# Performance work log

Measured on AMD Instinct MI355X. Metric: run time of the kernel, lower is better.

The kernel has to match this reference:

```python
import jax, jax.numpy as jnp
import numpy as np

NB_OBJECTS = 3
DIM_BODY = 10
DIM_OBJECT = 15
DIM_OBJ_FEAT = NB_OBJECTS + DIM_OBJECT  # 18
DIM_PHI_IN = 54
HID = 256
DIM_PHI_OUT = 256
DIM_RHO_OUT = 1
B = 65536

# (o1, o2) object pair and (j, k) predicate indices, as in the torch code
PAIRS = [((0, 1), (3, 5)), ((0, 2), (4, 7)), ((1, 2), (6, 8))]


def setup_inputs() -> dict:
    key = jax.random.key(0)
    ks = jax.random.split(key, 24)
    inp = {
        "obs": jax.random.normal(ks[0], (B, 55), dtype=jnp.float32),
        "ag": jax.random.uniform(ks[1], (B, 9), dtype=jnp.float32),
        "g": jax.random.uniform(ks[2], (B, 9), dtype=jnp.float32),
        "anchor_g": jax.random.uniform(ks[3], (B, 9), dtype=jnp.float32),
        "act": jax.random.normal(ks[4], (B, 4), dtype=jnp.float32),
    }
    s = 0.05
    # PhiCriticDeepSet: two independent 2-layer MLPs (streams 1 and 2)
    inp["w1"] = jax.random.normal(ks[5], (DIM_PHI_IN, HID), dtype=jnp.float32) * s
    inp["b1"] = jnp.zeros((HID,), dtype=jnp.float32)
    inp["w2"] = jax.random.normal(ks[6], (HID, DIM_PHI_OUT), dtype=jnp.float32) * s
    inp["b2"] = jnp.zeros((DIM_PHI_OUT,), dtype=jnp.float32)
    inp["w3"] = jax.random.normal(ks[7], (DIM_PHI_IN, HID), dtype=jnp.float32) * s
    inp["b3"] = jnp.zeros((HID,), dtype=jnp.float32)
    inp["w4"] = jax.random.normal(ks[8], (HID, DIM_PHI_OUT), dtype=jnp.float32) * s
    inp["b4"] = jnp.zeros((DIM_PHI_OUT,), dtype=jnp.float32)
    # RhoCriticDeepSet: two independent 2-layer heads
    inp["w5"] = jax.random.normal(ks[9], (DIM_PHI_OUT, HID), dtype=jnp.float32) * s
    inp["b5"] = jnp.zeros((HID,), dtype=jnp.float32)
    inp["w6"] = jax.random.normal(ks[10], (HID, DIM_RHO_OUT), dtype=jnp.float32) * s
    inp["b6"] = jnp.zeros((DIM_RHO_OUT,), dtype=jnp.float32)
    inp["w7"] = jax.random.normal(ks[11], (DIM_PHI_OUT, HID), dtype=jnp.float32) * s
    inp["b7"] = jnp.zeros((HID,), dtype=jnp.float32)
    inp["w8"] = jax.random.normal(ks[12], (HID, DIM_RHO_OUT), dtype=jnp.float32) * s
    inp["b8"] = jnp.zeros((DIM_RHO_OUT,), dtype=jnp.float32)
    return inp


def _build_pair_inputs(obs, ag, g, act, anchor_g):
    """combinations_trick branch: data-dependent gather of goal bits and object pairs."""
    bs = obs.shape[0]
    obs_body = obs[:, :DIM_BODY]
    eye = jnp.eye(NB_OBJECTS, dtype=obs.dtype)
    # obs_objects: [3, B, 18] = one-hot(3) ++ object state(15)
    obs_objects = jnp.stack([
        jnp.concatenate([jnp.broadcast_to(eye[i], (bs, NB_OBJECTS)),
                         obs[:, DIM_BODY + DIM_OBJECT * i: DIM_BODY + DIM_OBJECT * (i + 1)]],
                        axis=1)
        for i in range(NB_OBJECTS)], axis=0)
    bidx = jnp.arange(bs)
    inputs = []
    for i, ((o1, o2), (j, k)) in enumerate(PAIRS):
        # selector = anchor_g @ [e_j, e_k] difference = anchor_g[:, j] - anchor_g[:, k]
        sel = (anchor_g[:, j] - anchor_g[:, k]) >= 0  # [B] bool
        # idxs_bits[i] = [i, j] where sel else [i, k]
        bit2 = jnp.where(sel, j, k)  # [B] int
        ag_pair = jnp.stack([ag[:, i], ag[bidx, bit2]], axis=1)  # [B, 2]
        g_pair = jnp.stack([g[:, i], g[bidx, bit2]], axis=1)     # [B, 2]
        # idxs_objects[i] = [o1, o2] where sel else [o2, o1]
        oi = jnp.where(sel, o1, o2)  # [B]
        oj = jnp.where(sel, o2, o1)
        obj_first = obs_objects[oi, bidx]   # [B, 18] gather along object axis
        obj_second = obs_objects[oj, bidx]  # [B, 18]
        inputs.append(jnp.concatenate(
            [ag_pair, g_pair, obs_body, obj_first, obj_second, act], axis=1))
    return jnp.stack(inputs)  # [3, B, 54]


def reference(obs, ag, g, anchor_g, act,
              w1, b1, w2, b2, w3, b3, w4, b4,
              w5, b5, w6, b6, w7, b7, w8, b8):
    inp = _build_pair_inputs(obs, ag, g, act, anchor_g)  # [3, B, 54]
    # PhiCriticDeepSet (two relu-relu streams)
    x1 = jax.nn.relu(jnp.einsum('pbi,ih->pbh', jax.nn.relu(jnp.einsum('pbd,dh->pbh', inp, w1) + b1), w2) + b2)
    x2 = jax.nn.relu(jnp.einsum('pbi,ih->pbh', jax.nn.relu(jnp.einsum('pbd,dh->pbh', inp, w3) + b3), w4) + b4)
    s1 = x1.sum(axis=0)  # [B, 256] deepset sum over pairs
    s2 = x2.sum(axis=0)
    # RhoCriticDeepSet readouts
    q1 = jax.nn.relu(s1 @ w5 + b5) @ w6 + b6  # [B, 1]
    q2 = jax.nn.relu(s2 @ w7 + b7) @ w8 + b8  # [B, 1]
    return (q1, q2)
```

## Files before the change

### kernel.cpp

```cpp
#include <hip/hip_runtime.h>
#include <hip/hip_bf16.h>

typedef unsigned short u16;
typedef unsigned int   u32;

using bf8 = __attribute__((ext_vector_type(8))) __bf16;
using f4  = __attribute__((ext_vector_type(4))) float;

__device__ __forceinline__ float b2f(u16 u) {
    union { u32 i; float f; } v; v.i = ((u32)u) << 16; return v.f;
}
__device__ __forceinline__ u16 f2b(float f) {
    union { float f; u32 i; } v; v.f = f;
    u32 x = v.i;
    x += 0x7fffu + ((x >> 16) & 1u);
    return (u16)(x >> 16);
}
__device__ __forceinline__ u32 pk2(float lo, float hi) {
    union { __hip_bfloat162 h; u32 u; } v;
    v.h = __float22bfloat162_rn(make_float2(lo, hi));
    return v.u;
}

__global__ void swz_all(const float* __restrict__ w1, const float* __restrict__ w3,
                        const float* __restrict__ w2, const float* __restrict__ w4,
                        const float* __restrict__ w5, const float* __restrict__ w7,
                        u16* __restrict__ ws) {
    __shared__ u16 slab[32 * 270];
    int b = blockIdx.x, t = threadIdx.x;
    const float* src; u16* dst; int kmax, kt;
    if      (b <  2) { src = w1; dst = ws;          kmax = 54;  kt = b;      }
    else if (b <  4) { src = w3; dst = ws + 16384;  kmax = 54;  kt = b - 2;  }
    else if (b < 12) { src = w2; dst = ws + 32768;  kmax = 256; kt = b - 4;  }
    else if (b < 20) { src = w4; dst = ws + 98304;  kmax = 256; kt = b - 12; }
    else if (b < 28) { src = w5; dst = ws + 163840; kmax = 256; kt = b - 20; }
    else             { src = w7; dst = ws + 229376; kmax = 256; kt = b - 28; }

    #pragma unroll
    for (int it = 0; it < 8; ++it) {
        int flat = it * 1024 + t * 4;
        int row = flat >> 8, col = flat & 255;
        int k = kt * 32 + row;
        float4 v = make_float4(0.f, 0.f, 0.f, 0.f);
        if (k < kmax) v = *(const float4*)(src + k * 256 + col);
        u32* sp = (u32*)&slab[row * 270 + col];
        sp[0] = pk2(v.x, v.y);
        sp[1] = pk2(v.z, v.w);
    }
    __syncthreads();

    int lane = t & 63, wave = t >> 6, lr = lane & 15, kg = lane >> 4;
    #pragma unroll
    for (int i = 0; i < 4; ++i) {
        int ct = wave * 4 + i;
        u16 v[8];
        #pragma unroll
        for (int j = 0; j < 8; ++j)
            v[j] = slab[(kg * 8 + j) * 270 + ct * 16 + lr];
        uint4 o;
        o.x = (u32)v[0] | ((u32)v[1] << 16);
        o.y = (u32)v[2] | ((u32)v[3] << 16);
        o.z = (u32)v[4] | ((u32)v[5] << 16);
        o.w = (u32)v[6] | ((u32)v[7] << 16);
        *(uint4*)(dst + (size_t)(((kt * 16 + ct) * 64 + lane) * 8)) = o;
    }
}

#define HS    264
#define H_OFF 3456
#define S2O   (16 * HS)
#define RH0O  (32 * HS)

__global__ __launch_bounds__(256, 2) void critic_kernel(
    const float* __restrict__ obs, const float* __restrict__ ag,
    const float* __restrict__ g,   const float* __restrict__ anchor,
    const float* __restrict__ act,
    const float* __restrict__ b1,  const float* __restrict__ b2,
    const float* __restrict__ b3,  const float* __restrict__ b4,
    const float* __restrict__ b5,  const float* __restrict__ b7,
    const float* __restrict__ w6,  const float* __restrict__ b6,
    const float* __restrict__ w8,  const float* __restrict__ b8,
    const u16* __restrict__ wsz, float* __restrict__ out, int B) {

    __shared__ u16 pool[H_OFF + 48 * HS];

    const int t    = threadIdx.x;
    const int lane = t & 63;
    const int wave = t >> 6;
    const int lr   = lane & 15;
    const int lg   = lane >> 4;
    const int wg   = blockIdx.x;

    if (t < 48) {
        const int O1[3] = {0, 0, 1}, O2[3] = {1, 2, 2};
        const int JA[3] = {3, 4, 6}, KA[3] = {5, 7, 8};
        int p = t / 16, bl = t % 16;
        int b = wg * 16 + bl;
        int j = JA[p], k = KA[p];
        bool sel = (anchor[b * 9 + j] - anchor[b * 9 + k]) >= 0.0f;
        int bit2 = sel ? j : k;
        int oi = sel ? O1[p] : O2[p];
        int oj = sel ? O2[p] : O1[p];
        u16* row = &pool[t * 72];
        row[0] = f2b(ag[b * 9 + p]);
        row[1] = f2b(ag[b * 9 + bit2]);
        row[2] = f2b(g[b * 9 + p]);
        row[3] = f2b(g[b * 9 + bit2]);
        for (int c = 0; c < 10; ++c) row[4 + c] = f2b(obs[b * 55 + c]);
        const u16 ONE = 0x3F80;
        row[14] = (oi == 0) ? ONE : 0; row[15] = (oi == 1) ? ONE : 0; row[16] = (oi == 2) ? ONE : 0;
        for (int c = 0; c < 15; ++c) row[17 + c] = f2b(obs[b * 55 + 10 + 15 * oi + c]);
        row[32] = (oj == 0) ? ONE : 0; row[33] = (oj == 1) ? ONE : 0; row[34] = (oj == 2) ? ONE : 0;
        for (int c = 0; c < 15; ++c) row[35 + c] = f2b(obs[b * 55 + 10 + 15 * oj + c]);
        for (int c = 0; c < 4; ++c)  row[50 + c] = f2b(act[b * 4 + c]);
        for (int c = 54; c < 64; ++c) row[c] = 0;
    }
    __syncthreads();

    u32 s1w[4][2];
    u32 s2w[4][2];

    for (int net = 0; net < 2; ++net) {
        const u16* Wl1 = wsz + (net ? 16384 : 0);
        const u16* Wl2 = wsz + 32768 + (net ? 65536 : 0);
        const float* bl1 = net ? b3 : b1;
        const float* bl2 = net ? b4 : b2;

        f4 acc[3][4];
        #pragma unroll
        for (int rt = 0; rt < 3; ++rt)
            #pragma unroll
            for (int c = 0; c < 4; ++c) acc[rt][c] = (f4){0.f, 0.f, 0.f, 0.f};
        #pragma unroll
        for (int kt = 0; kt < 2; ++kt) {
            bf8 wfr[4];
            #pragma unroll
            for (int c = 0; c < 4; ++c)
                wfr[c] = *(const bf8*)(Wl1 + (size_t)(((kt * 16 + wave * 4 + c) * 64 + lane) * 8));
            #pragma unroll
            for (int rt = 0; rt < 3; ++rt) {
                bf8 xfr = *(const bf8*)(&pool[(rt * 16 + lr) * 72 + kt * 32 + lg * 8]);
                #pragma unroll
                for (int c = 0; c < 4; ++c)
                    acc[rt][c] = __builtin_amdgcn_mfma_f32_16x16x32_bf16(wfr[c], xfr, acc[rt][c], 0, 0, 0);
            }
        }
        #pragma unroll
        for (int c = 0; c < 4; ++c) {
            float4 bv = *(const float4*)(bl1 + (wave * 4 + c) * 16 + lg * 4);
            #pragma unroll
            for (int rt = 0; rt < 3; ++rt) {
                uint2 w;
                w.x = pk2(fmaxf(acc[rt][c][0] + bv.x, 0.f), fmaxf(acc[rt][c][1] + bv.y, 0.f));
                w.y = pk2(fmaxf(acc[rt][c][2] + bv.z, 0.f), fmaxf(acc[rt][c][3] + bv.w, 0.f));
                *(uint2*)&pool[H_OFF + (rt * 16 + lr) * HS + (wave * 4 + c) * 16 + lg * 4] = w;
            }
        }
        __syncthreads();

        f4 acc2[3][4];
        #pragma unroll
        for (int rt = 0; rt < 3; ++rt)
            #pragma unroll
            for (int c = 0; c < 4; ++c) acc2[rt][c] = (f4){0.f, 0.f, 0.f, 0.f};
        #pragma unroll
        for (int ks = 0; ks < 8; ++ks) {
            bf8 wfr[4];
            #pragma unroll
            for (int c = 0; c < 4; ++c)
                wfr[c] = *(const bf8*)(Wl2 + (size_t)(((ks * 16 + wave * 4 + c) * 64 + lane) * 8));
            #pragma unroll
            for (int rt = 0; rt < 3; ++rt) {
                bf8 hfr = *(const bf8*)(&pool[H_OFF + (rt * 16 + lr) * HS + ks * 32 + lg * 8]);
                #pragma unroll
                for (int c = 0; c < 4; ++c)
                    acc2[rt][c] = __builtin_amdgcn_mfma_f32_16x16x32_bf16(wfr[c], hfr, acc2[rt][c], 0, 0, 0);
            }
        }
        #pragma unroll
        for (int c = 0; c < 4; ++c) {
            float4 bv = *(const float4*)(bl2 + (wave * 4 + c) * 16 + lg * 4);
            f4 sv = (f4){0.f, 0.f, 0.f, 0.f};
            #pragma unroll
            for (int p = 0; p < 3; ++p) {
                sv[0] += fmaxf(acc2[p][c][0] + bv.x, 0.f);
                sv[1] += fmaxf(acc2[p][c][1] + bv.y, 0.f);
                sv[2] += fmaxf(acc2[p][c][2] + bv.z, 0.f);
                sv[3] += fmaxf(acc2[p][c][3] + bv.w, 0.f);
            }
            if (net == 0) {
                s1w[c][0] = pk2(sv[0], sv[1]);
                s1w[c][1] = pk2(sv[2], sv[3]);
            } else {
                s2w[c][0] = pk2(sv[0], sv[1]);
                s2w[c][1] = pk2(sv[2], sv[3]);
            }
        }
        __syncthreads();
    }

    #pragma unroll
    for (int c = 0; c < 4; ++c) {
        int base = H_OFF + lr * HS + (wave * 4 + c) * 16 + lg * 4;
        *(uint2*)&pool[base]       = *(uint2*)&s1w[c][0];
        *(uint2*)&pool[base + S2O] = *(uint2*)&s2w[c][0];
    }
    __syncthreads();

    {
        const u16* W5 = wsz + 163840;
        const u16* W7 = wsz + 229376;
        f4 racc[2][4];
        #pragma unroll
        for (int rt = 0; rt < 2; ++rt)
            #pragma unroll
            for (int c = 0; c < 4; ++c) racc[rt][c] = (f4){0.f, 0.f, 0.f, 0.f};
        #pragma unroll
        for (int ks = 0; ks < 8; ++ks) {
            bf8 w5f[4], w7f[4];
            #pragma unroll
            for (int c = 0; c < 4; ++c) {
                size_t off = (size_t)(((ks * 16 + wave * 4 + c) * 64 + lane) * 8);
                w5f[c] = *(const bf8*)(W5 + off);
                w7f[c] = *(const bf8*)(W7 + off);
            }
            bf8 s1f = *(const bf8*)(&pool[H_OFF + lr * HS + ks * 32 + lg * 8]);
            bf8 s2f = *(const bf8*)(&pool[H_OFF + S2O + lr * HS + ks * 32 + lg * 8]);
            #pragma unroll
            for (int c = 0; c < 4; ++c) {
                racc[0][c] = __builtin_amdgcn_mfma_f32_16x16x32_bf16(w5f[c], s1f, racc[0][c], 0, 0, 0);
                racc[1][c] = __builtin_amdgcn_mfma_f32_16x16x32_bf16(w7f[c], s2f, racc[1][c], 0, 0, 0);
            }
        }
        #pragma unroll
        for (int c = 0; c < 4; ++c) {
            float4 bv = *(const float4*)(b5 + (wave * 4 + c) * 16 + lg * 4);
            uint2 w;
            w.x = pk2(fmaxf(racc[0][c][0] + bv.x, 0.f), fmaxf(racc[0][c][1] + bv.y, 0.f));
            w.y = pk2(fmaxf(racc[0][c][2] + bv.z, 0.f), fmaxf(racc[0][c][3] + bv.w, 0.f));
            *(uint2*)&pool[H_OFF + RH0O + lr * HS + (wave * 4 + c) * 16 + lg * 4] = w;
        }
        __syncthreads();
        #pragma unroll
        for (int c = 0; c < 4; ++c) {
            float4 bv = *(const float4*)(b7 + (wave * 4 + c) * 16 + lg * 4);
            uint2 w;
            w.x = pk2(fmaxf(racc[1][c][0] + bv.x, 0.f), fmaxf(racc[1][c][1] + bv.y, 0.f));
            w.y = pk2(fmaxf(racc[1][c][2] + bv.z, 0.f), fmaxf(racc[1][c][3] + bv.w, 0.f));
            *(uint2*)&pool[H_OFF + lr * HS + (wave * 4 + c) * 16 + lg * 4] = w;
        }
        __syncthreads();
    }

    {
        int oidx = t & 31;
        int kc   = t >> 5;
        int net  = oidx >> 4, r = oidx & 15;
        int hoff = net ? H_OFF : H_OFF + RH0O;
        const float* wv = net ? w8 : w6;
        float s = 0.f;
        int base = hoff + r * HS + kc * 32;
        #pragma unroll
        for (int it = 0; it < 8; ++it) {
            uint2 two = *(const uint2*)&pool[base + it * 4];
            float4 wq = *(const float4*)(wv + kc * 32 + it * 4);
            s += __uint_as_float(two.x << 16)          * wq.x;
            s += __uint_as_float(two.x & 0xffff0000u)  * wq.y;
            s += __uint_as_float(two.y << 16)          * wq.z;
            s += __uint_as_float(two.y & 0xffff0000u)  * wq.w;
        }
        __syncthreads();
        ((u32*)pool)[t] = __float_as_uint(s);
    }
    __syncthreads();
    if (t < 32) {
        int net = t >> 4, r = t & 15;
        float qv = net ? b8[0] : b6[0];
        #pragma unroll
        for (int kc = 0; kc < 8; ++kc)
            qv += __uint_as_float(((u32*)pool)[kc * 32 + t]);
        out[net * B + wg * 16 + r] = qv;
    }
}

extern "C" void kernel_launch(void* const* d_in, const int* in_sizes, int n_in,
                              void* d_out, int out_size, void* d_ws, size_t ws_size,
                              hipStream_t stream) {
    const float* obs = (const float*)d_in[0];
    const float* ag  = (const float*)d_in[1];
    const float* g   = (const float*)d_in[2];
    const float* anc = (const float*)d_in[3];
    const float* act = (const float*)d_in[4];
    const float* w1  = (const float*)d_in[5];
    const float* b1  = (const float*)d_in[6];
    const float* w2  = (const float*)d_in[7];
    const float* b2  = (const float*)d_in[8];
    const float* w3  = (const float*)d_in[9];
    const float* b3  = (const float*)d_in[10];
    const float* w4  = (const float*)d_in[11];
    const float* b4  = (const float*)d_in[12];
    const float* w5  = (const float*)d_in[13];
    const float* b5  = (const float*)d_in[14];
    const float* w6  = (const float*)d_in[15];
    const float* b6  = (const float*)d_in[16];
    const float* w7  = (const float*)d_in[17];
    const float* b7  = (const float*)d_in[18];
    const float* w8  = (const float*)d_in[19];
    const float* b8  = (const float*)d_in[20];
    u16* ws    = (u16*)d_ws;
    float* out = (float*)d_out;
    int B = in_sizes[0] / 55;

    swz_all<<<36, 256, 0, stream>>>(w1, w3, w2, w4, w5, w7, ws);
    critic_kernel<<<(B + 15) / 16, 256, 0, stream>>>(obs, ag, g, anc, act,
                                                     b1, b2, b3, b4, b5, b7,
                                                     w6, b6, w8, b8, ws, out, B);
}
```

Before: 228.4 us.

## Process two 16-row batch tiles per block with software-pipelined stages

Each workgroup now handles 32 batch rows as two 16-row halves and interleaves their stages (layer1 of one half with layer2 of the other, rho with dot products) across shared barriers. This halves the number of barriers per row and lets independent MFMA work from two tiles overlap with LDS writes and global weight fetches. The cost is roughly double the LDS footprint and more live registers, which may reduce occupancy under the 2-blocks launch bound, and half as many blocks are launched.

```diff
diff --git a/kernel.cpp b/kernel.cpp
--- a/kernel.cpp
+++ b/kernel.cpp
@@ -66,10 +66,166 @@
     }
 }
 
-#define HS    264
-#define H_OFF 3456
-#define S2O   (16 * HS)
-#define RH0O  (32 * HS)
+#define HS   264
+#define HA   6912
+#define HB   19584
+
+__device__ __forceinline__ void do_l1(u16* pool, int lane, int wave, int lr, int lg,
+                                      const u16* W, const float* bias,
+                                      int inpOff, int hOff) {
+    f4 acc[3][4];
+    #pragma unroll
+    for (int rt = 0; rt < 3; ++rt)
+        #pragma unroll
+        for (int c = 0; c < 4; ++c) acc[rt][c] = (f4){0.f, 0.f, 0.f, 0.f};
+    #pragma unroll
+    for (int kt = 0; kt < 2; ++kt) {
+        bf8 wfr[4];
+        #pragma unroll
+        for (int c = 0; c < 4; ++c)
+            wfr[c] = *(const bf8*)(W + (size_t)(((kt * 16 + wave * 4 + c) * 64 + lane) * 8));
+        #pragma unroll
+        for (int rt = 0; rt < 3; ++rt) {
+            bf8 xfr = *(const bf8*)(&pool[inpOff + (rt * 16 + lr) * 72 + kt * 32 + lg * 8]);
+            #pragma unroll
+            for (int c = 0; c < 4; ++c)
+                acc[rt][c] = __builtin_amdgcn_mfma_f32_16x16x32_bf16(wfr[c], xfr, acc[rt][c], 0, 0, 0);
+        }
+    }
+    #pragma unroll
+    for (int c = 0; c < 4; ++c) {
+        float4 bv = *(const float4*)(bias + (wave * 4 + c) * 16 + lg * 4);
+        #pragma unroll
+        for (int rt = 0; rt < 3; ++rt) {
+            uint2 w;
+            w.x = pk2(fmaxf(acc[rt][c][0] + bv.x, 0.f), fmaxf(acc[rt][c][1] + bv.y, 0.f));
+            w.y = pk2(fmaxf(acc[rt][c][2] + bv.z, 0.f), fmaxf(acc[rt][c][3] + bv.w, 0.f));
+            *(uint2*)&pool[hOff + (rt * 16 + lr) * HS + (wave * 4 + c) * 16 + lg * 4] = w;
+        }
+    }
+}
+
+__device__ __forceinline__ void do_l2(u16* pool, int lane, int wave, int lr, int lg,
+                                      const u16* W, const float* bias,
+                                      int hOff, u32 sw[4][2]) {
+    f4 acc2[3][4];
+    #pragma unroll
+    for (int rt = 0; rt < 3; ++rt)
+        #pragma unroll
+        for (int c = 0; c < 4; ++c) acc2[rt][c] = (f4){0.f, 0.f, 0.f, 0.f};
+    #pragma unroll
+    for (int ks = 0; ks < 8; ++ks) {
+        bf8 wfr[4];
+        #pragma unroll
+        for (int c = 0; c < 4; ++c)
+            wfr[c] = *(const bf8*)(W + (size_t)(((ks * 16 + wave * 4 + c) * 64 + lane) * 8));
+        #pragma unroll
+        for (int rt = 0; rt < 3; ++rt) {
+            bf8 hfr = *(const bf8*)(&pool[hOff + (rt * 16 + lr) * HS + ks * 32 + lg * 8]);
+            #pragma unroll
+            for (int c = 0; c < 4; ++c)
+                acc2[rt][c] = __builtin_amdgcn_mfma_f32_16x16x32_bf16(wfr[c], hfr, acc2[rt][c], 0, 0, 0);
+        }
+    }
+    #pragma unroll
+    for (int c = 0; c < 4; ++c) {
+        float4 bv = *(const float4*)(bias + (wave * 4 + c) * 16 + lg * 4);
+        f4 sv = (f4){0.f, 0.f, 0.f, 0.f};
+        #pragma unroll
+        for (int p = 0; p < 3; ++p) {
+            sv[0] += fmaxf(acc2[p][c][0] + bv.x, 0.f);
+            sv[1] += fmaxf(acc2[p][c][1] + bv.y, 0.f);
+            sv[2] += fmaxf(acc2[p][c][2] + bv.z, 0.f);
+            sv[3] += fmaxf(acc2[p][c][3] + bv.w, 0.f);
+        }
+        sw[c][0] = pk2(sv[0], sv[1]);
+        sw[c][1] = pk2(sv[2], sv[3]);
+    }
+}
+
+__device__ __forceinline__ void do_swrite(u16* pool, int wave, int lr, int lg,
+                                          int sOff, u32 s1[4][2], u32 s2[4][2]) {
+    #pragma unroll
+    for (int c = 0; c < 4; ++c) {
+        int base = sOff + lr * HS + (wave * 4 + c) * 16 + lg * 4;
+        *(uint2*)&pool[base]           = *(uint2*)&s1[c][0];
+        *(uint2*)&pool[base + 16 * HS] = *(uint2*)&s2[c][0];
+    }
+}
+
+__device__ __forceinline__ void do_rho(u16* pool, int lane, int wave, int lr, int lg,
+                                       const u16* W5, const u16* W7,
+                                       const float* b5, const float* b7,
+                                       int sOff, int rh0Off, int rh1Off) {
+    f4 racc[2][4];
+    #pragma unroll
+    for (int rt = 0; rt < 2; ++rt)
+        #pragma unroll
+        for (int c = 0; c < 4; ++c) racc[rt][c] = (f4){0.f, 0.f, 0.f, 0.f};
+    #pragma unroll
+    for (int ks = 0; ks < 8; ++ks) {
+        bf8 w5f[4], w7f[4];
+        #pragma unroll
+        for (int c = 0; c < 4; ++c) {
+            size_t off = (size_t)(((ks * 16 + wave * 4 + c) * 64 + lane) * 8);
+            w5f[c] = *(const bf8*)(W5 + off);
+            w7f[c] = *(const bf8*)(W7 + off);
+        }
+        bf8 s1f = *(const bf8*)(&pool[sOff + lr * HS + ks * 32 + lg * 8]);
+        bf8 s2f = *(const bf8*)(&pool[sOff + 16 * HS + lr * HS + ks * 32 + lg * 8]);
+        #pragma unroll
+        for (int c = 0; c < 4; ++c) {
+            racc[0][c] = __builtin_amdgcn_mfma_f32_16x16x32_bf16(w5f[c], s1f, racc[0][c], 0, 0, 0);
+            racc[1][c] = __builtin_amdgcn_mfma_f32_16x16x32_bf16(w7f[c], s2f, racc[1][c], 0, 0, 0);
+        }
+    }
+    #pragma unroll
+    for (int c = 0; c < 4; ++c) {
+        float4 bv5 = *(const float4*)(b5 + (wave * 4 + c) * 16 + lg * 4);
+        float4 bv7 = *(const float4*)(b7 + (wave * 4 + c) * 16 + lg * 4);
+        uint2 w0, w1;
+        w0.x = pk2(fmaxf(racc[0][c][0] + bv5.x, 0.f), fmaxf(racc[0][c][1] + bv5.y, 0.f));
+        w0.y = pk2(fmaxf(racc[0][c][2] + bv5.z, 0.f), fmaxf(racc[0][c][3] + bv5.w, 0.f));
+        w1.x = pk2(fmaxf(racc[1][c][0] + bv7.x, 0.f), fmaxf(racc[1][c][1] + bv7.y, 0.f));
+        w1.y = pk2(fmaxf(racc[1][c][2] + bv7.z, 0.f), fmaxf(racc[1][c][3] + bv7.w, 0.f));
+        int col = (wave * 4 + c) * 16 + lg * 4;
+        *(uint2*)&pool[rh0Off + lr * HS + col] = w0;
+        *(uint2*)&pool[rh1Off + lr * HS + col] = w1;
+    }
+}
+
+__device__ __forceinline__ void do_dotpart(u16* pool, int t,
+                                           const float* w6, const float* w8,
+                                           int rh0Off, int rh1Off, int partOff) {
+    int oidx = t & 31, kc = t >> 5;
+    int net = oidx >> 4, r = oidx & 15;
+    const float* wv = net ? w8 : w6;
+    int base = (net ? rh1Off : rh0Off) + r * HS + kc * 32;
+    float s = 0.f;
+    #pragma unroll
+    for (int it = 0; it < 8; ++it) {
+        uint2 two = *(const uint2*)&pool[base + it * 4];
+        float4 wq = *(const float4*)(wv + kc * 32 + it * 4);
+        s += __uint_as_float(two.x << 16)          * wq.x;
+        s += __uint_as_float(two.x & 0xffff0000u)  * wq.y;
+        s += __uint_as_float(two.y << 16)          * wq.z;
+        s += __uint_as_float(two.y & 0xffff0000u)  * wq.w;
+    }
+    ((u32*)pool)[partOff + t] = __float_as_uint(s);
+}
+
+__device__ __forceinline__ void do_out(u16* pool, int t,
+                                       const float* b6, const float* b8,
+                                       int partOff, float* out, int bbase, int B) {
+    if (t < 32) {
+        int net = t >> 4, r = t & 15;
+        float qv = net ? b8[0] : b6[0];
+        #pragma unroll
+        for (int kc = 0; kc < 8; ++kc)
+            qv += __uint_as_float(((u32*)pool)[partOff + kc * 32 + t]);
+        out[net * B + bbase + r] = qv;
+    }
+}
 
 __global__ __launch_bounds__(256, 2) void critic_kernel(
     const float* __restrict__ obs, const float* __restrict__ ag,
@@ -82,7 +238,7 @@
     const float* __restrict__ w8,  const float* __restrict__ b8,
     const u16* __restrict__ wsz, float* __restrict__ out, int B) {
 
-    __shared__ u16 pool[H_OFF + 48 * HS];
+    __shared__ u16 pool[6912 + 96 * HS];
 
     const int t    = threadIdx.x;
     const int lane = t & 63;
@@ -91,17 +247,26 @@
     const int lg   = lane >> 4;
     const int wg   = blockIdx.x;
 
-    if (t < 48) {
+    const u16* W1n0 = wsz;
+    const u16* W1n1 = wsz + 16384;
+    const u16* W2n0 = wsz + 32768;
+    const u16* W2n1 = wsz + 98304;
+    const u16* W5   = wsz + 163840;
+    const u16* W7   = wsz + 229376;
+
+    if (t < 96) {
         const int O1[3] = {0, 0, 1}, O2[3] = {1, 2, 2};
         const int JA[3] = {3, 4, 6}, KA[3] = {5, 7, 8};
-        int p = t / 16, bl = t % 16;
-        int b = wg * 16 + bl;
+        int half = t >= 48;
+        int loc = t - half * 48;
+        int p = loc / 16, bl = loc % 16;
+        int b = wg * 32 + half * 16 + bl;
         int j = JA[p], k = KA[p];
         bool sel = (anchor[b * 9 + j] - anchor[b * 9 + k]) >= 0.0f;
         int bit2 = sel ? j : k;
         int oi = sel ? O1[p] : O2[p];
         int oj = sel ? O2[p] : O1[p];
-        u16* row = &pool[t * 72];
+        u16* row = &pool[half * 3456 + loc * 72];
         row[0] = f2b(ag[b * 9 + p]);
         row[1] = f2b(ag[b * 9 + bit2]);
         row[2] = f2b(g[b * 9 + p]);
@@ -117,170 +282,40 @@
     }
     __syncthreads();
 
-    u32 s1w[4][2];
-    u32 s2w[4][2];
-
-    for (int net = 0; net < 2; ++net) {
-        const u16* Wl1 = wsz + (net ? 16384 : 0);
-        const u16* Wl2 = wsz + 32768 + (net ? 65536 : 0);
-        const float* bl1 = net ? b3 : b1;
-        const float* bl2 = net ? b4 : b2;
-
-        f4 acc[3][4];
-        #pragma unroll
-        for (int rt = 0; rt < 3; ++rt)
-            #pragma unroll
-            for (int c = 0; c < 4; ++c) acc[rt][c] = (f4){0.f, 0.f, 0.f, 0.f};
-        #pragma unroll
-        for (int kt = 0; kt < 2; ++kt) {
-            bf8 wfr[4];
-            #pragma unroll
-            for (int c = 0; c < 4; ++c)
-                wfr[c] = *(const bf8*)(Wl1 + (size_t)(((kt * 16 + wave * 4 + c) * 64 + lane) * 8));
-            #pragma unroll
-            for (int rt = 0; rt < 3; ++rt) {
-                bf8 xfr = *(const bf8*)(&pool[(rt * 16 + lr) * 72 + kt * 32 + lg * 8]);
-                #pragma unroll
-                for (int c = 0; c < 4; ++c)
-                    acc[rt][c] = __builtin_amdgcn_mfma_f32_16x16x32_bf16(wfr[c], xfr, acc[rt][c], 0, 0, 0);
-            }
-        }
-        #pragma unroll
-        for (int c = 0; c < 4; ++c) {
-            float4 bv = *(const float4*)(bl1 + (wave * 4 + c) * 16 + lg * 4);
-            #pragma unroll
-            for (int rt = 0; rt < 3; ++rt) {
-                uint2 w;
-                w.x = pk2(fmaxf(acc[rt][c][0] + bv.x, 0.f), fmaxf(acc[rt][c][1] + bv.y, 0.f));
-                w.y = pk2(fmaxf(acc[rt][c][2] + bv.z, 0.f), fmaxf(acc[rt][c][3] + bv.w, 0.f));
-                *(uint2*)&pool[H_OFF + (rt * 16 + lr) * HS + (wave * 4 + c) * 16 + lg * 4] = w;
-            }
-        }
-        __syncthreads();
-
-        f4 acc2[3][4];
-        #pragma unroll
-        for (int rt = 0; rt < 3; ++rt)
-            #pragma unroll
-            for (int c = 0; c < 4; ++c) acc2[rt][c] = (f4){0.f, 0.f, 0.f, 0.f};
-        #pragma unroll
-        for (int ks = 0; ks < 8; ++ks) {
-            bf8 wfr[4];
-            #pragma unroll
-            for (int c = 0; c < 4; ++c)
-                wfr[c] = *(const bf8*)(Wl2 + (size_t)(((ks * 16 + wave * 4 + c) * 64 + lane) * 8));
-            #pragma unroll
-            for (int rt = 0; rt < 3; ++rt) {
-                bf8 hfr = *(const bf8*)(&pool[H_OFF + (rt * 16 + lr) * HS + ks * 32 + lg * 8]);
-                #pragma unroll
-                for (int c = 0; c < 4; ++c)
-                    acc2[rt][c] = __builtin_amdgcn_mfma_f32_16x16x32_bf16(wfr[c], hfr, acc2[rt][c], 0, 0, 0);
-            }
-        }
-        #pragma unroll
-        for (int c = 0; c < 4; ++c) {
-            float4 bv = *(const float4*)(bl2 + (wave * 4 + c) * 16 + lg * 4);
-            f4 sv = (f4){0.f, 0.f, 0.f, 0.f};
-            #pragma unroll
-            for (int p = 0; p < 3; ++p) {
-                sv[0] += fmaxf(acc2[p][c][0] + bv.x, 0.f);
-                sv[1] += fmaxf(acc2[p][c][1] + bv.y, 0.f);
-                sv[2] += fmaxf(acc2[p][c][2] + bv.z, 0.f);
-                sv[3] += fmaxf(acc2[p][c][3] + bv.w, 0.f);
-            }
-            if (net == 0) {
-                s1w[c][0] = pk2(sv[0], sv[1]);
-                s1w[c][1] = pk2(sv[2], sv[3]);
-            } else {
-                s2w[c][0] = pk2(sv[0], sv[1]);
-                s2w[c][1] = pk2(sv[2], sv[3]);
-            }
-        }
-        __syncthreads();
-    }
-
-    #pragma unroll
-    for (int c = 0; c < 4; ++c) {
-        int base = H_OFF + lr * HS + (wave * 4 + c) * 16 + lg * 4;
-        *(uint2*)&pool[base]       = *(uint2*)&s1w[c][0];
-        *(uint2*)&pool[base + S2O] = *(uint2*)&s2w[c][0];
-    }
-    __syncthreads();
-
-    {
-        const u16* W5 = wsz + 163840;
-        const u16* W7 = wsz + 229376;
-        f4 racc[2][4];
-        #pragma unroll
-        for (int rt = 0; rt < 2; ++rt)
-            #pragma unroll
-            for (int c = 0; c < 4; ++c) racc[rt][c] = (f4){0.f, 0.f, 0.f, 0.f};
-        #pragma unroll
-        for (int ks = 0; ks < 8; ++ks) {
-            bf8 w5f[4], w7f[4];
-            #pragma unroll
-            for (int c = 0; c < 4; ++c) {
-                size_t off = (size_t)(((ks * 16 + wave * 4 + c) * 64 + lane) * 8);
-                w5f[c] = *(const bf8*)(W5 + off);
-                w7f[c] = *(const bf8*)(W7 + off);
-            }
-            bf8 s1f = *(const bf8*)(&pool[H_OFF + lr * HS + ks * 32 + lg * 8]);
-            bf8 s2f = *(const bf8*)(&pool[H_OFF + S2O + lr * HS + ks * 32 + lg * 8]);
-            #pragma unroll
-            for (int c = 0; c < 4; ++c) {
-                racc[0][c] = __builtin_amdgcn_mfma_f32_16x16x32_bf16(w5f[c], s1f, racc[0][c], 0, 0, 0);
-                racc[1][c] = __builtin_amdgcn_mfma_f32_16x16x32_bf16(w7f[c], s2f, racc[1][c], 0, 0, 0);
-            }
-        }
-        #pragma unroll
-        for (int c = 0; c < 4; ++c) {
-            float4 bv = *(const float4*)(b5 + (wave * 4 + c) * 16 + lg * 4);
-            uint2 w;
-            w.x = pk2(fmaxf(racc[0][c][0] + bv.x, 0.f), fmaxf(racc[0][c][1] + bv.y, 0.f));
-            w.y = pk2(fmaxf(racc[0][c][2] + bv.z, 0.f), fmaxf(racc[0][c][3] + bv.w, 0.f));
-            *(uint2*)&pool[H_OFF + RH0O + lr * HS + (wave * 4 + c) * 16 + lg * 4] = w;
-        }
-        __syncthreads();
-        #pragma unroll
-        for (int c = 0; c < 4; ++c) {
-            float4 bv = *(const float4*)(b7 + (wave * 4 + c) * 16 + lg * 4);
-            uint2 w;
-            w.x = pk2(fmaxf(racc[1][c][0] + bv.x, 0.f), fmaxf(racc[1][c][1] + bv.y, 0.f));
-            w.y = pk2(fmaxf(racc[1][c][2] + bv.z, 0.f), fmaxf(racc[1][c][3] + bv.w, 0.f));
-            *(uint2*)&pool[H_OFF + lr * HS + (wave * 4 + c) * 16 + lg * 4] = w;
-        }
-        __syncthreads();
-    }
-
-    {
-        int oidx = t & 31;
-        int kc   = t >> 5;
-        int net  = oidx >> 4, r = oidx & 15;
-        int hoff = net ? H_OFF : H_OFF + RH0O;
-        const float* wv = net ? w8 : w6;
-        float s = 0.f;
-        int base = hoff + r * HS + kc * 32;
-        #pragma unroll
-        for (int it = 0; it < 8; ++it) {
-            uint2 two = *(const uint2*)&pool[base + it * 4];
-            float4 wq = *(const float4*)(wv + kc * 32 + it * 4);
-            s += __uint_as_float(two.x << 16)          * wq.x;
-            s += __uint_as_float(two.x & 0xffff0000u)  * wq.y;
-            s += __uint_as_float(two.y << 16)          * wq.z;
-            s += __uint_as_float(two.y & 0xffff0000u)  * wq.w;
-        }
-        __syncthreads();
-        ((u32*)pool)[t] = __float_as_uint(s);
-    }
-    __syncthreads();
-    if (t < 32) {
-        int net = t >> 4, r = t & 15;
-        float qv = net ? b8[0] : b6[0];
-        #pragma unroll
-        for (int kc = 0; kc < 8; ++kc)
-            qv += __uint_as_float(((u32*)pool)[kc * 32 + t]);
-        out[net * B + wg * 16 + r] = qv;
-    }
+    u32 s1wA[4][2], s2wA[4][2], s1wB[4][2], s2wB[4][2];
+
+    do_l1(pool, lane, wave, lr, lg, W1n0, b1, 0, HA);
+    __syncthreads();
+
+    do_l2(pool, lane, wave, lr, lg, W2n0, b2, HA, s1wA);
+    do_l1(pool, lane, wave, lr, lg, W1n0, b1, 3456, HB);
+    __syncthreads();
+
+    do_l1(pool, lane, wave, lr, lg, W1n1, b3, 0, HA);
+    do_l2(pool, lane, wave, lr, lg, W2n0, b2, HB, s1wB);
+    __syncthreads();
+
+    do_l2(pool, lane, wave, lr, lg, W2n1, b4, HA, s2wA);
+    do_l1(pool, lane, wave, lr, lg, W1n1, b3, 3456, HB);
+    __syncthreads();
+
+    do_swrite(pool, wave, lr, lg, HA, s1wA, s2wA);
+    do_l2(pool, lane, wave, lr, lg, W2n1, b4, HB, s2wB);
+    __syncthreads();
+
+    do_rho(pool, lane, wave, lr, lg, W5, W7, b5, b7, HA, HA + 32 * HS, 0);
+    do_swrite(pool, wave, lr, lg, HB, s1wB, s2wB);
+    __syncthreads();
+
+    do_dotpart(pool, t, w6, w8, HA + 32 * HS, 0, 2112);
+    do_rho(pool, lane, wave, lr, lg, W5, W7, b5, b7, HB, HB + 32 * HS, HA);
+    __syncthreads();
+
+    do_out(pool, t, b6, b8, 2112, out, wg * 32, B);
+    do_dotpart(pool, t, w6, w8, HB + 32 * HS, HA, 2368);
+    __syncthreads();
+
+    do_out(pool, t, b6, b8, 2368, out, wg * 32 + 16, B);
 }
 
 extern "C" void kernel_launch(void* const* d_in, const int* in_sizes, int n_in,
@@ -312,7 +347,7 @@
     int B = in_sizes[0] / 55;
 
     swz_all<<<36, 256, 0, stream>>>(w1, w3, w2, w4, w5, w7, ws);
-    critic_kernel<<<(B + 15) / 16, 256, 0, stream>>>(obs, ag, g, anc, act,
+    critic_kernel<<<(B + 31) / 32, 256, 0, stream>>>(obs, ag, g, anc, act,
                                                      b1, b2, b3, b4, b5, b7,
                                                      w6, b6, w8, b8, ws, out, B);
 }
```

New measurement: 222.6 us. -2.6%, faster.
